# Kernel optimization log

Hardware: AMD Instinct MI355X
Metric: run time of the kernel (lower is better)

## Reference

```python
import jax, jax.numpy as jnp
import numpy as np

EPS = 1e-8
K_KNN = 20

def vn_lin(W, x):
    # W: [Cout, Cin], x: [B, Cin, 3, ...] -> [B, Cout, 3, ...]
    return jnp.einsum('oi,bi...->bo...', W, x)

def vn_relu(Wd, x):
    # VNLeakyReLU with negative_slope=0, share_nonlinearity=False
    d = jnp.einsum('oi,bi...->bo...', Wd, x)
    dot = jnp.sum(x * d, axis=2, keepdims=True)   # sum over 3-vector axis
    dsq = jnp.sum(d * d, axis=2, keepdims=True) + EPS
    return jnp.where(dot >= 0, x, x - (dot / dsq) * d)

def graph_feature_cross(p, k):
    # p: [B, N, 3] -> feat: [B, 3, 3, N, k]
    xx = jnp.sum(p * p, axis=-1)                       # [B,N]
    inner = jnp.einsum('bnd,bmd->bnm', p, p)           # [B,N,N]
    neg_dist = 2.0 * inner - xx[:, :, None] - xx[:, None, :]
    idx = jax.lax.top_k(neg_dist, k)[1]                # [B,N,k] nearest neighbors
    nbrs = jax.vmap(lambda pb, ib: pb[ib])(p, idx)     # [B,N,k,3]
    xr = jnp.broadcast_to(p[:, :, None, :], nbrs.shape)
    cross = jnp.cross(nbrs, xr)                        # [B,N,k,3]
    feat = jnp.stack([nbrs - xr, xr, cross], axis=3)   # [B,N,k,3(ch),3(vec)]
    return jnp.transpose(feat, (0, 3, 4, 1, 2))        # [B,3,3,N,k]

def setup_inputs() -> dict:
    key = jax.random.key(0)
    ks = jax.random.split(key, 9)
    B, N = 4, 2048
    H = 128           # hidden_dim // 3
    C_IN = 2 * H      # 256
    CC = 128          # c_dim // 3
    s_in = 1.0 / np.sqrt(C_IN)
    s_h = 1.0 / np.sqrt(H)
    return {
        'p': jax.random.normal(ks[0], (B, N, 3), dtype=jnp.float32),
        'fc_pos_W': jax.random.normal(ks[1], (C_IN, 3), dtype=jnp.float32) / np.sqrt(3.0),
        'blk_d0': jax.random.normal(ks[2], (5, C_IN, C_IN), dtype=jnp.float32) * s_in,
        'blk_W0': jax.random.normal(ks[3], (5, H, C_IN), dtype=jnp.float32) * s_in,
        'blk_d1': jax.random.normal(ks[4], (5, H, H), dtype=jnp.float32) * s_h,
        'blk_W1': jax.random.normal(ks[5], (5, H, H), dtype=jnp.float32) * s_h,
        'blk_Ws': jax.random.normal(ks[6], (5, H, C_IN), dtype=jnp.float32) * s_in,
        'fc_c_W': jax.random.normal(ks[7], (CC, H), dtype=jnp.float32) * s_h,
        'act_d': jax.random.normal(ks[8], (H, H), dtype=jnp.float32) * s_h,
    }

def reference(p, fc_pos_W, blk_d0, blk_W0, blk_d1, blk_W1, blk_Ws, fc_c_W, act_d):
    feat = graph_feature_cross(p, K_KNN)          # [B,3,3,N,k]
    x = vn_lin(fc_pos_W, feat)                    # [B,256,3,N,k]
    net = jnp.mean(x, axis=-1)                    # mean_pool over k -> [B,256,3,N]

    def block(i, x):
        h = vn_lin(blk_W0[i], vn_relu(blk_d0[i], x))
        dx = vn_lin(blk_W1[i], vn_relu(blk_d1[i], h))
        return vn_lin(blk_Ws[i], x) + dx          # shortcut (size_in != size_out)

    net = block(0, net)                           # [B,128,3,N]
    for i in range(1, 5):
        pooled = jnp.broadcast_to(jnp.mean(net, axis=3, keepdims=True), net.shape)
        net = block(i, jnp.concatenate([net, pooled], axis=1))
    net = jnp.mean(net, axis=3)                   # [B,128,3]
    c = vn_lin(fc_c_W, vn_relu(act_d, net))       # [B,128,3]
    return c.reshape(c.shape[0], -1)              # [B,384]
```

## Files before the change

kernel.cpp:

```cpp
#include <hip/hip_runtime.h>
#include <math.h>

#define N_PTS 2048
#define K_NN  20
#define K_D   10
#define WTOT  819200

typedef unsigned short u16;
typedef unsigned int   u32;
typedef _Float16 f16;
using half8   = __attribute__((ext_vector_type(8))) _Float16;
using floatx4 = __attribute__((ext_vector_type(4))) float;

__device__ __forceinline__ void split2h(float v, f16& h, f16& l) {
    h = (f16)v;
    l = (f16)((v - (float)h) * 1024.0f);
}

__device__ __forceinline__ float neg_dist(float4 q2, float4 c) {
    return fmaf(q2.x, c.x, fmaf(q2.y, c.y, fmaf(q2.z, c.z, -q2.w))) - c.w;
}

__global__ __launch_bounds__(256) void prep_kernel(
    const float* __restrict__ pts, float* __restrict__ m_out,
    const float* __restrict__ bd0, const float* __restrict__ bW0,
    const float* __restrict__ bd1, const float* __restrict__ bW1,
    const float* __restrict__ bWs, u16* __restrict__ Wswz,
    float* __restrict__ nm_acc)
{
    __shared__ float4 sp[N_PTS];
    if (blockIdx.x >= 1024) {
        int i = (blockIdx.x - 1024) * 256 + threadIdx.x;
        if (i >= WTOT) return;
        if (i < 7680) nm_acc[i] = 0.f;
        float v; int base, K, local;
        if (i < 327680)      { int rel = i;          base = (rel/65536)*65536;            local = rel%65536; K = 256; v = bd0[rel]; }
        else if (i < 491520) { int rel = i - 327680; base = 327680 + (rel/32768)*32768;   local = rel%32768; K = 256; v = bW0[rel]; }
        else if (i < 573440) { int rel = i - 491520; base = 491520 + (rel/16384)*16384;   local = rel%16384; K = 128; v = bd1[rel]; }
        else if (i < 655360) { int rel = i - 573440; base = 573440 + (rel/16384)*16384;   local = rel%16384; K = 128; v = bW1[rel]; }
        else                 { int rel = i - 655360; base = 655360 + (rel/32768)*32768;   local = rel%32768; K = 256; v = bWs[rel]; }
        int m = local / K, k = local % K;
        int NKF = K >> 5;
        int mf = m >> 4, r = m & 15;
        int kf = k >> 5, q = (k >> 3) & 3, ii = k & 7;
        int lane = q*16 + r;
        int dst = base + ((mf*NKF + kf)*64 + lane)*8 + ii;
        f16 h, l; split2h(v, h, l);
        f16* W = (f16*)Wswz;
        W[dst] = h; W[WTOT + dst] = l;
        return;
    }

    const int b     = blockIdx.x >> 8;
    const int qbase = (blockIdx.x & 255) << 3;
    const int ql    = threadIdx.x >> 5;
    const int sl    = threadIdx.x & 31;
    const float* pb = pts + (size_t)b * N_PTS * 3;
    for (int i = threadIdx.x; i < N_PTS; i += 256) {
        float x = pb[i*3+0], y = pb[i*3+1], z = pb[i*3+2];
        sp[i] = make_float4(x, y, z, x*x + y*y + z*z);
    }
    __syncthreads();

    const int n = qbase + ql;
    const float4 q = sp[n];
    const float4 q2 = make_float4(2.f*q.x, 2.f*q.y, 2.f*q.z, q.w);

    float t[K_D];
#pragma unroll
    for (int s = 0; s < K_D; ++s) t[s] = -INFINITY;

    for (int j = 0; j < N_PTS/32; ++j) {
        float4 c = sp[j*32 + sl];
        float v = neg_dist(q2, c);
#pragma unroll
        for (int s = 0; s < K_D; ++s) {
            float nx = (s < K_D-1) ? t[s+1] : INFINITY;
            t[s] = fminf(fmaxf(t[s], v), nx);
        }
    }

    float head = t[K_D-1];
    float T = -INFINITY;
#pragma unroll 1
    for (int e = 0; e < K_NN; ++e) {
        float v = head; int w = sl;
#pragma unroll
        for (int off = 1; off < 32; off <<= 1) {
            float vo = __shfl_xor(v, off);
            int   wo = __shfl_xor(w, off);
            bool take = (vo > v) || (vo == v && wo < w);
            v = take ? vo : v;
            w = take ? wo : w;
        }
        T = v;
        if (w == sl) {
#pragma unroll
            for (int s = K_D-1; s > 0; --s) t[s] = t[s-1];
            t[0] = -INFINITY;
            head = t[K_D-1];
        }
    }

    float sx = 0.f, sy = 0.f, sz = 0.f;
    for (int j = 0; j < N_PTS/32; ++j) {
        float4 c = sp[j*32 + sl];
        float v = neg_dist(q2, c);
        if (v >= T) { sx += c.x; sy += c.y; sz += c.z; }
    }
#pragma unroll
    for (int off = 1; off < 32; off <<= 1) {
        sx += __shfl_xor(sx, off);
        sy += __shfl_xor(sy, off);
        sz += __shfl_xor(sz, off);
    }
    if (sl == 0) {
        const float inv = 1.0f / (float)K_NN;
        const int pt = b * N_PTS + n;
        m_out[pt*3+0] = sx * inv;
        m_out[pt*3+1] = sy * inv;
        m_out[pt*3+2] = sz * inv;
    }
}

template<int MF, int JF>
__device__ __forceinline__ void run_gemm_split(
    const f16* __restrict__ Whi, const f16* __restrict__ Wlo, size_t aoff,
    int NKF, int NK, const f16* Blds, int bstride, int lane,
    floatx4 (&acc)[MF][JF], floatx4 (&accL)[MF][JF])
{
    const int l15 = lane & 15;
    const int lq8 = (lane >> 4) * 8;
    half8 Aa[2*MF], Ab[2*MF];

    auto loada = [&](half8* dst, int kf) {
#pragma unroll
        for (int fm = 0; fm < MF; ++fm) {
            size_t fo = aoff + (size_t)(fm*NKF + kf)*512 + (size_t)lane*8;
            dst[fm*2+0] = *(const half8*)(Whi + fo);
            dst[fm*2+1] = *(const half8*)(Wlo + fo);
        }
    };
    auto step = [&](half8* af, int kf) {
        half8 bq[JF];
#pragma unroll
        for (int fj = 0; fj < JF; ++fj)
            bq[fj] = *(const half8*)&Blds[(fj*16 + l15)*bstride + kf*32 + lq8];
#pragma unroll
        for (int fm = 0; fm < MF; ++fm)
#pragma unroll
            for (int fj = 0; fj < JF; ++fj) {
                acc[fm][fj]  = __builtin_amdgcn_mfma_f32_16x16x32_f16(af[fm*2+0], bq[fj], acc[fm][fj], 0, 0, 0);
                accL[fm][fj] = __builtin_amdgcn_mfma_f32_16x16x32_f16(af[fm*2+1], bq[fj], accL[fm][fj], 0, 0, 0);
            }
    };

    loada(Aa, 0);
#pragma unroll 1
    for (int kf = 0; kf < NK; kf += 2) {
        loada(Ab, kf + 1);
        step(Aa, kf);
        if (kf + 2 < NK) loada(Aa, kf + 2);
        step(Ab, kf + 1);
    }
}

template<int MF, int JF>
__device__ __forceinline__ void run_gemm_hi(
    const f16* __restrict__ Whi, size_t aoff,
    int NKF, int NK, const f16* Blds, int bstride, int lane,
    floatx4 (&acc)[MF][JF])
{
    const int l15 = lane & 15;
    const int lq8 = (lane >> 4) * 8;
    half8 Aa[MF], Ab[MF];

    auto loada = [&](half8* dst, int kf) {
#pragma unroll
        for (int fm = 0; fm < MF; ++fm) {
            size_t fo = aoff + (size_t)(fm*NKF + kf)*512 + (size_t)lane*8;
            dst[fm] = *(const half8*)(Whi + fo);
        }
    };
    auto step = [&](half8* af, int kf) {
        half8 bq[JF];
#pragma unroll
        for (int fj = 0; fj < JF; ++fj)
            bq[fj] = *(const half8*)&Blds[(fj*16 + l15)*bstride + kf*32 + lq8];
#pragma unroll
        for (int fm = 0; fm < MF; ++fm)
#pragma unroll
            for (int fj = 0; fj < JF; ++fj)
                acc[fm][fj] = __builtin_amdgcn_mfma_f32_16x16x32_f16(af[fm], bq[fj], acc[fm][fj], 0, 0, 0);
    };

    loada(Aa, 0);
#pragma unroll 1
    for (int kf = 0; kf < NK; kf += 2) {
        loada(Ab, kf + 1);
        step(Aa, kf);
        if (kf + 2 < NK) loada(Aa, kf + 2);
        step(Ab, kf + 1);
    }
}

__device__ __forceinline__ uint2 pack_res(floatx4 a, floatx4 aL) {
    u16 hh[4];
#pragma unroll
    for (int r = 0; r < 4; ++r) {
        f16 hv = (f16)(a[r] + aL[r] * (1.0f/1024.0f));
        hh[r] = *(u16*)&hv;
    }
    uint2 pv;
    pv.x = (u32)hh[0] | ((u32)hh[1] << 16);
    pv.y = (u32)hh[2] | ((u32)hh[3] << 16);
    return pv;
}

__device__ __forceinline__ uint2 pack_hi(floatx4 a) {
    u16 hh[4];
#pragma unroll
    for (int r = 0; r < 4; ++r) {
        f16 hv = (f16)a[r];
        hh[r] = *(u16*)&hv;
    }
    uint2 pv;
    pv.x = (u32)hh[0] | ((u32)hh[1] << 16);
    pv.y = (u32)hh[2] | ((u32)hh[3] << 16);
    return pv;
}

__global__ __launch_bounds__(256, 2) void resblk_kernel(
    const u16* __restrict__ Wswz,
    int offD0, int offW0, int offD1, int offW1, int offWs,
    const f16* __restrict__ netIn, const float* __restrict__ nm_prev,
    const float* __restrict__ pts, const float* __restrict__ m_buf,
    const float* __restrict__ fcW,
    f16* __restrict__ netOut, float* __restrict__ nm_out, int blk0)
{
    __shared__ struct {
        f16 X[48*264];
        union { f16 d[48*264]; float C[48*132]; } Y;
        f16 H[48*136];
    } s;

    const int tid  = threadIdx.x;
    const int jb   = blockIdx.x * 48;
    const int bB   = blockIdx.x >> 7;
    const int lane = tid & 63;
    const int wv   = tid >> 6;
    const f16* Whi = (const f16*)Wswz;
    const f16* Wlo = Whi + WTOT;

    if (blk0) {
        float* Hf = (float*)s.H;
        const int ptbase = blockIdx.x * 16;
        for (int i = tid; i < 768; i += 256) Hf[i] = fcW[i];
        if (tid < 96) Hf[768 + tid] = (tid < 48) ? pts[ptbase*3 + tid]
                                                 : m_buf[ptbase*3 + tid - 48];
        __syncthreads();
#pragma unroll 1
        for (int it = 0; it < 6; ++it) {
            int idx = tid + 256*it;
            int r = idx >> 5;
            int cg = idx & 31;
            int l = r / 3, v = r - l*3;
            float p0 = Hf[768+l*3], p1 = Hf[768+l*3+1], p2 = Hf[768+l*3+2];
            float m0 = Hf[816+l*3], m1 = Hf[816+l*3+1], m2 = Hf[816+l*3+2];
            float pv[3] = {p0,p1,p2}, mv[3] = {m0,m1,m2};
            int v1 = (v==2) ? 0 : v+1;
            int v2 = (v==0) ? 2 : v-1;
            float av = mv[v] - pv[v];
            float bv = pv[v];
            float cv = mv[v1]*pv[v2] - mv[v2]*pv[v1];
            half8 o;
#pragma unroll
            for (int k = 0; k < 8; ++k) {
                int ch = cg*8 + k;
                o[k] = (f16)(Hf[ch*3+0]*av + Hf[ch*3+1]*bv + Hf[ch*3+2]*cv);
            }
            *(half8*)&s.X[r*264 + cg*8] = o;
        }
    } else {
#pragma unroll 1
        for (int it = 0; it < 6; ++it) {
            int idx = tid + 256*it;
            int r = idx >> 5;
            int cg = idx & 31;
            if (cg < 16) {
                uint4 vv = *(const uint4*)(netIn + (size_t)(jb + r)*128 + cg*8);
                *(uint4*)&s.X[r*264 + cg*8] = vv;
            } else {
                int v = r % 3;
                const float* np = nm_prev + (bB*3+v)*128 + (cg-16)*8;
                half8 o;
#pragma unroll
                for (int k = 0; k < 8; ++k) o[k] = (f16)(np[k] * (1.0f/2048.0f));
                *(half8*)&s.X[r*264 + cg*8] = o;
            }
        }
    }
    __syncthreads();

    {
        floatx4 acc[4][3];
#pragma unroll
        for (int a = 0; a < 4; ++a)
#pragma unroll
            for (int b = 0; b < 3; ++b) acc[a][b] = (floatx4){0,0,0,0};
        run_gemm_hi<4,3>(Whi, (size_t)offD0 + (size_t)wv*16384, 8, 8, s.X, 264, lane, acc);
#pragma unroll
        for (int fm = 0; fm < 4; ++fm)
#pragma unroll
            for (int fj = 0; fj < 3; ++fj) {
                int mloc = wv*64 + fm*16 + (lane>>4)*4;
                int jl   = fj*16 + (lane & 15);
                *(uint2*)&s.Y.d[jl*264 + mloc] = pack_hi(acc[fm][fj]);
            }
    }
    __syncthreads();

#pragma unroll 1
    for (int it = 0; it < 2; ++it) {
        int idx = tid + 256*it;
        int l = idx >> 5, cg = idx & 31;
        half8 xa = *(const half8*)&s.X[(l*3+0)*264 + cg*8];
        half8 xb = *(const half8*)&s.X[(l*3+1)*264 + cg*8];
        half8 xc = *(const half8*)&s.X[(l*3+2)*264 + cg*8];
        half8 da = *(const half8*)&s.Y.d[(l*3+0)*264 + cg*8];
        half8 db = *(const half8*)&s.Y.d[(l*3+1)*264 + cg*8];
        half8 dc = *(const half8*)&s.Y.d[(l*3+2)*264 + cg*8];
        half8 ya, yb, yc;
#pragma unroll
        for (int k = 0; k < 8; ++k) {
            float x0 = (float)xa[k], x1 = (float)xb[k], x2 = (float)xc[k];
            float d0 = (float)da[k], d1 = (float)db[k], d2 = (float)dc[k];
            float dot = x0*d0 + x1*d1 + x2*d2;
            float y0, y1, y2;
            if (dot >= 0.f) { y0 = x0; y1 = x1; y2 = x2; }
            else {
                float dsq = d0*d0 + d1*d1 + d2*d2 + 1e-8f;
                float sc = dot / dsq;
                y0 = x0 - sc*d0; y1 = x1 - sc*d1; y2 = x2 - sc*d2;
            }
            ya[k] = (f16)y0; yb[k] = (f16)y1; yc[k] = (f16)y2;
        }
        *(half8*)&s.Y.d[(l*3+0)*264 + cg*8] = ya;
        *(half8*)&s.Y.d[(l*3+1)*264 + cg*8] = yb;
        *(half8*)&s.Y.d[(l*3+2)*264 + cg*8] = yc;
    }
    __syncthreads();

    {
        floatx4 acc[2][3], accL[2][3];
#pragma unroll
        for (int a = 0; a < 2; ++a)
#pragma unroll
            for (int b = 0; b < 3; ++b) { acc[a][b] = (floatx4){0,0,0,0}; accL[a][b] = (floatx4){0,0,0,0}; }
        run_gemm_split<2,3>(Whi, Wlo, (size_t)offW0 + (size_t)wv*8192, 8, 8, s.Y.d, 264, lane, acc, accL);
#pragma unroll
        for (int fm = 0; fm < 2; ++fm)
#pragma unroll
            for (int fj = 0; fj < 3; ++fj) {
                int mloc = wv*32 + fm*16 + (lane>>4)*4;
                int jl   = fj*16 + (lane & 15);
                *(uint2*)&s.H[jl*136 + mloc] = pack_res(acc[fm][fj], accL[fm][fj]);
            }
    }
    __syncthreads();

    {
        floatx4 acc[2][3];
#pragma unroll
        for (int a = 0; a < 2; ++a)
#pragma unroll
            for (int b = 0; b < 3; ++b) acc[a][b] = (floatx4){0,0,0,0};
        run_gemm_hi<2,3>(Whi, (size_t)offD1 + (size_t)wv*4096, 4, 4, s.H, 136, lane, acc);
#pragma unroll
        for (int fm = 0; fm < 2; ++fm)
#pragma unroll
            for (int fj = 0; fj < 3; ++fj) {
                int mloc = wv*32 + fm*16 + (lane>>4)*4;
                int jl   = fj*16 + (lane & 15);
                *(uint2*)&s.Y.d[jl*136 + mloc] = pack_hi(acc[fm][fj]);
            }
    }
    __syncthreads();

    {
        int l = tid >> 4, cg = tid & 15;
        half8 xa = *(const half8*)&s.H[(l*3+0)*136 + cg*8];
        half8 xb = *(const half8*)&s.H[(l*3+1)*136 + cg*8];
        half8 xc = *(const half8*)&s.H[(l*3+2)*136 + cg*8];
        half8 da = *(const half8*)&s.Y.d[(l*3+0)*136 + cg*8];
        half8 db = *(const half8*)&s.Y.d[(l*3+1)*136 + cg*8];
        half8 dc = *(const half8*)&s.Y.d[(l*3+2)*136 + cg*8];
        half8 ya, yb, yc;
#pragma unroll
        for (int k = 0; k < 8; ++k) {
            float x0 = (float)xa[k], x1 = (float)xb[k], x2 = (float)xc[k];
            float d0 = (float)da[k], d1 = (float)db[k], d2 = (float)dc[k];
            float dot = x0*d0 + x1*d1 + x2*d2;
            float y0, y1, y2;
            if (dot >= 0.f) { y0 = x0; y1 = x1; y2 = x2; }
            else {
                float dsq = d0*d0 + d1*d1 + d2*d2 + 1e-8f;
                float sc = dot / dsq;
                y0 = x0 - sc*d0; y1 = x1 - sc*d1; y2 = x2 - sc*d2;
            }
            ya[k] = (f16)y0; yb[k] = (f16)y1; yc[k] = (f16)y2;
        }
        __syncthreads();
        *(half8*)&s.H[(l*3+0)*136 + cg*8] = ya;
        *(half8*)&s.H[(l*3+1)*136 + cg*8] = yb;
        *(half8*)&s.H[(l*3+2)*136 + cg*8] = yc;
    }
    __syncthreads();

    {
        floatx4 acc[2][3], accL[2][3];
#pragma unroll
        for (int a = 0; a < 2; ++a)
#pragma unroll
            for (int b = 0; b < 3; ++b) { acc[a][b] = (floatx4){0,0,0,0}; accL[a][b] = (floatx4){0,0,0,0}; }
        run_gemm_split<2,3>(Whi, Wlo, (size_t)offWs + (size_t)wv*8192, 8, 8, s.X, 264, lane, acc, accL);
        run_gemm_split<2,3>(Whi, Wlo, (size_t)offW1 + (size_t)wv*4096, 4, 4, s.H, 136, lane, acc, accL);
#pragma unroll
        for (int fm = 0; fm < 2; ++fm)
#pragma unroll
            for (int fj = 0; fj < 3; ++fj) {
                int mloc = wv*32 + fm*16 + (lane>>4)*4;
                int jl   = fj*16 + (lane & 15);
                floatx4 res;
#pragma unroll
                for (int r = 0; r < 4; ++r) res[r] = acc[fm][fj][r] + accL[fm][fj][r] * (1.0f/1024.0f);
                u16 hh[4];
#pragma unroll
                for (int r = 0; r < 4; ++r) { f16 hv = (f16)res[r]; hh[r] = *(u16*)&hv; }
                uint2 pv;
                pv.x = (u32)hh[0] | ((u32)hh[1] << 16);
                pv.y = (u32)hh[2] | ((u32)hh[3] << 16);
                *(uint2*)(netOut + (size_t)(jb + jl)*128 + mloc) = pv;
                *(floatx4*)&s.Y.C[jl*132 + mloc] = res;
            }
    }
    __syncthreads();

#pragma unroll 1
    for (int idx = tid; idx < 384; idx += 256) {
        int v = idx >> 7, ch = idx & 127;
        float sum = 0.f;
#pragma unroll 1
        for (int pt = 0; pt < 16; ++pt) sum += s.Y.C[(pt*3+v)*132 + ch];
        atomicAdd(nm_out + (bB*3+v)*128 + ch, sum);
    }
}

__global__ __launch_bounds__(128) void final_kernel(const float* __restrict__ nm_sum,
                                                    const float* __restrict__ act_d,
                                                    const float* __restrict__ fc_c,
                                                    float* __restrict__ out)
{
    const int b = blockIdx.x;
    const int c = threadIdx.x;
    __shared__ float xs[128][3];
    __shared__ float ys[128][3];
    xs[c][0] = nm_sum[(b*3+0)*128 + c] * (1.0f/2048.0f);
    xs[c][1] = nm_sum[(b*3+1)*128 + c] * (1.0f/2048.0f);
    xs[c][2] = nm_sum[(b*3+2)*128 + c] * (1.0f/2048.0f);
    __syncthreads();
    float d0 = 0.f, d1 = 0.f, d2 = 0.f;
    for (int i = 0; i < 128; ++i) {
        float w = act_d[c*128 + i];
        d0 = fmaf(w, xs[i][0], d0);
        d1 = fmaf(w, xs[i][1], d1);
        d2 = fmaf(w, xs[i][2], d2);
    }
    float x0 = xs[c][0], x1 = xs[c][1], x2 = xs[c][2];
    float dot = x0*d0 + x1*d1 + x2*d2;
    float y0, y1, y2;
    if (dot >= 0.f) { y0 = x0; y1 = x1; y2 = x2; }
    else {
        float dsq = d0*d0 + d1*d1 + d2*d2 + 1e-8f;
        float sc = dot / dsq;
        y0 = x0 - sc*d0; y1 = x1 - sc*d1; y2 = x2 - sc*d2;
    }
    ys[c][0] = y0; ys[c][1] = y1; ys[c][2] = y2;
    __syncthreads();
    float o0 = 0.f, o1 = 0.f, o2 = 0.f;
    for (int i = 0; i < 128; ++i) {
        float w = fc_c[c*128 + i];
        o0 = fmaf(w, ys[i][0], o0);
        o1 = fmaf(w, ys[i][1], o1);
        o2 = fmaf(w, ys[i][2], o2);
    }
    out[b*384 + c*3 + 0] = o0;
    out[b*384 + c*3 + 1] = o1;
    out[b*384 + c*3 + 2] = o2;
}

extern "C" void kernel_launch(void* const* d_in, const int* in_sizes, int n_in,
                              void* d_out, int out_size, void* d_ws, size_t ws_size,
                              hipStream_t stream)
{
    const float* p      = (const float*)d_in[0];
    const float* fc_pos = (const float*)d_in[1];
    const float* bd0    = (const float*)d_in[2];
    const float* bW0    = (const float*)d_in[3];
    const float* bd1    = (const float*)d_in[4];
    const float* bW1    = (const float*)d_in[5];
    const float* bWs    = (const float*)d_in[6];
    const float* fc_c   = (const float*)d_in[7];
    const float* act_d  = (const float*)d_in[8];
    float* out = (float*)d_out;

    char* w = (char*)d_ws;
    float* m_buf  = (float*)w;  w += 98304;
    float* nm_acc = (float*)w;  w += 5*1536*4;
    u16*   Wswz   = (u16*)w;    w += (size_t)2*WTOT*2;
    f16*   netA   = (f16*)w;    w += (size_t)24576*128*2;
    f16*   netB   = (f16*)w;    w += (size_t)24576*128*2;

    prep_kernel<<<dim3(1024 + 3200), dim3(256), 0, stream>>>(
        p, m_buf, bd0, bW0, bd1, bW1, bWs, Wswz, nm_acc);

    f16* nIn = netA;
    f16* nOut = netB;
    for (int blk = 0; blk < 5; ++blk) {
        const int offD0 = blk*65536;
        const int offW0 = 327680 + blk*32768;
        const int offD1 = 491520 + blk*16384;
        const int offW1 = 573440 + blk*16384;
        const int offWs = 655360 + blk*32768;
        const float* nmp = (blk == 0) ? nullptr : (nm_acc + (blk-1)*1536);
        resblk_kernel<<<dim3(512), dim3(256), 0, stream>>>(
            Wswz, offD0, offW0, offD1, offW1, offWs,
            (blk == 0) ? netA : nIn, nmp, p, m_buf, fc_pos,
            nOut, nm_acc + blk*1536, (blk == 0) ? 1 : 0);
        f16* tmp = nIn; nIn = nOut; nOut = tmp;
    }

    final_kernel<<<dim3(4), dim3(128), 0, stream>>>(nm_acc + 4*1536, act_d, fc_c, out);

    (void)in_sizes; (void)n_in; (void)out_size; (void)ws_size;
}
```

Before: 242.4 us.

## Fuse final head into last resblock via last-block counter; triple-buffer GEMM loads

The separate final_kernel launch is removed. The last resblock kernel now uses an atomic completion counter so the final block to finish computes the VN-ReLU and linear head, and that launch also skips writing netOut, which nothing reads. The GEMM helpers take K-depth as a template parameter, are fully unrolled, and use a three-deep register buffer for the weight fragments in place of two alternating buffers. The aim is to cut one launch and its gap, drop a global store, and hide weight-load latency better. The cost is a serialized tail in a single block, extra register pressure from the deeper buffer, and reliance on a threadfence/atomic pattern for correctness.

New measurement: 286.4 us. +18.2%, slower.

```diff
diff --git a/kernel.cpp b/kernel.cpp
--- a/kernel.cpp
+++ b/kernel.cpp
@@ -26,13 +26,14 @@
     const float* __restrict__ bd0, const float* __restrict__ bW0,
     const float* __restrict__ bd1, const float* __restrict__ bW1,
     const float* __restrict__ bWs, u16* __restrict__ Wswz,
-    float* __restrict__ nm_acc)
+    float* __restrict__ nm_acc, int* __restrict__ sync_cnt)
 {
     __shared__ float4 sp[N_PTS];
     if (blockIdx.x >= 1024) {
         int i = (blockIdx.x - 1024) * 256 + threadIdx.x;
         if (i >= WTOT) return;
         if (i < 7680) nm_acc[i] = 0.f;
+        if (i == 0) sync_cnt[0] = 0;
         float v; int base, K, local;
         if (i < 327680)      { int rel = i;          base = (rel/65536)*65536;            local = rel%65536; K = 256; v = bd0[rel]; }
         else if (i < 491520) { int rel = i - 327680; base = 327680 + (rel/32768)*32768;   local = rel%32768; K = 256; v = bW0[rel]; }
@@ -123,25 +124,61 @@
     }
 }
 
-template<int MF, int JF>
+template<int MF, int JF, int NK>
+__device__ __forceinline__ void run_gemm_hi(
+    const f16* __restrict__ Whi, size_t aoff,
+    const f16* Blds, int bstride, int lane,
+    floatx4 (&acc)[MF][JF])
+{
+    const int l15 = lane & 15;
+    const int lq8 = (lane >> 4) * 8;
+    half8 buf[3][MF];
+
+    auto loada = [&](half8 (&dst)[MF], int kf) {
+#pragma unroll
+        for (int fm = 0; fm < MF; ++fm)
+            dst[fm] = *(const half8*)(Whi + aoff + (size_t)(fm*NK + kf)*512 + (size_t)lane*8);
+    };
+    auto step = [&](half8 (&af)[MF], int kf) {
+        half8 bq[JF];
+#pragma unroll
+        for (int fj = 0; fj < JF; ++fj)
+            bq[fj] = *(const half8*)&Blds[(fj*16 + l15)*bstride + kf*32 + lq8];
+#pragma unroll
+        for (int fm = 0; fm < MF; ++fm)
+#pragma unroll
+            for (int fj = 0; fj < JF; ++fj)
+                acc[fm][fj] = __builtin_amdgcn_mfma_f32_16x16x32_f16(af[fm], bq[fj], acc[fm][fj], 0, 0, 0);
+    };
+
+    loada(buf[0], 0);
+    if (NK > 1) loada(buf[1], 1);
+#pragma unroll
+    for (int kf = 0; kf < NK; ++kf) {
+        if (kf + 2 < NK) loada(buf[(kf+2)%3], kf+2);
+        step(buf[kf%3], kf);
+    }
+}
+
+template<int MF, int JF, int NK>
 __device__ __forceinline__ void run_gemm_split(
     const f16* __restrict__ Whi, const f16* __restrict__ Wlo, size_t aoff,
-    int NKF, int NK, const f16* Blds, int bstride, int lane,
+    const f16* Blds, int bstride, int lane,
     floatx4 (&acc)[MF][JF], floatx4 (&accL)[MF][JF])
 {
     const int l15 = lane & 15;
     const int lq8 = (lane >> 4) * 8;
-    half8 Aa[2*MF], Ab[2*MF];
-
-    auto loada = [&](half8* dst, int kf) {
+    half8 buf[3][2*MF];
+
+    auto loada = [&](half8 (&dst)[2*MF], int kf) {
 #pragma unroll
         for (int fm = 0; fm < MF; ++fm) {
-            size_t fo = aoff + (size_t)(fm*NKF + kf)*512 + (size_t)lane*8;
+            size_t fo = aoff + (size_t)(fm*NK + kf)*512 + (size_t)lane*8;
             dst[fm*2+0] = *(const half8*)(Whi + fo);
             dst[fm*2+1] = *(const half8*)(Wlo + fo);
         }
     };
-    auto step = [&](half8* af, int kf) {
+    auto step = [&](half8 (&af)[2*MF], int kf) {
         half8 bq[JF];
 #pragma unroll
         for (int fj = 0; fj < JF; ++fj)
@@ -155,52 +192,12 @@
             }
     };
 
-    loada(Aa, 0);
-#pragma unroll 1
-    for (int kf = 0; kf < NK; kf += 2) {
-        loada(Ab, kf + 1);
-        step(Aa, kf);
-        if (kf + 2 < NK) loada(Aa, kf + 2);
-        step(Ab, kf + 1);
-    }
-}
-
-template<int MF, int JF>
-__device__ __forceinline__ void run_gemm_hi(
-    const f16* __restrict__ Whi, size_t aoff,
-    int NKF, int NK, const f16* Blds, int bstride, int lane,
-    floatx4 (&acc)[MF][JF])
-{
-    const int l15 = lane & 15;
-    const int lq8 = (lane >> 4) * 8;
-    half8 Aa[MF], Ab[MF];
-
-    auto loada = [&](half8* dst, int kf) {
-#pragma unroll
-        for (int fm = 0; fm < MF; ++fm) {
-            size_t fo = aoff + (size_t)(fm*NKF + kf)*512 + (size_t)lane*8;
-            dst[fm] = *(const half8*)(Whi + fo);
-        }
-    };
-    auto step = [&](half8* af, int kf) {
-        half8 bq[JF];
-#pragma unroll
-        for (int fj = 0; fj < JF; ++fj)
-            bq[fj] = *(const half8*)&Blds[(fj*16 + l15)*bstride + kf*32 + lq8];
-#pragma unroll
-        for (int fm = 0; fm < MF; ++fm)
-#pragma unroll
-            for (int fj = 0; fj < JF; ++fj)
-                acc[fm][fj] = __builtin_amdgcn_mfma_f32_16x16x32_f16(af[fm], bq[fj], acc[fm][fj], 0, 0, 0);
-    };
-
-    loada(Aa, 0);
-#pragma unroll 1
-    for (int kf = 0; kf < NK; kf += 2) {
-        loada(Ab, kf + 1);
-        step(Aa, kf);
-        if (kf + 2 < NK) loada(Aa, kf + 2);
-        step(Ab, kf + 1);
+    loada(buf[0], 0);
+    if (NK > 1) loada(buf[1], 1);
+#pragma unroll
+    for (int kf = 0; kf < NK; ++kf) {
+        if (kf + 2 < NK) loada(buf[(kf+2)%3], kf+2);
+        step(buf[kf%3], kf);
     }
 }
 
@@ -236,13 +233,17 @@
     const f16* __restrict__ netIn, const float* __restrict__ nm_prev,
     const float* __restrict__ pts, const float* __restrict__ m_buf,
     const float* __restrict__ fcW,
-    f16* __restrict__ netOut, float* __restrict__ nm_out, int blk0)
+    f16* __restrict__ netOut, float* __restrict__ nm_out, int blk0,
+    int do_head, int* __restrict__ sync_cnt,
+    const float* __restrict__ act_d, const float* __restrict__ fc_c,
+    float* __restrict__ out)
 {
     __shared__ struct {
         f16 X[48*264];
         union { f16 d[48*264]; float C[48*132]; } Y;
         f16 H[48*136];
     } s;
+    __shared__ int lastFlag;
 
     const int tid  = threadIdx.x;
     const int jb   = blockIdx.x * 48;
@@ -265,14 +266,13 @@
             int r = idx >> 5;
             int cg = idx & 31;
             int l = r / 3, v = r - l*3;
-            float p0 = Hf[768+l*3], p1 = Hf[768+l*3+1], p2 = Hf[768+l*3+2];
-            float m0 = Hf[816+l*3], m1 = Hf[816+l*3+1], m2 = Hf[816+l*3+2];
-            float pv[3] = {p0,p1,p2}, mv[3] = {m0,m1,m2};
+            float pv0[3] = {Hf[768+l*3], Hf[768+l*3+1], Hf[768+l*3+2]};
+            float mv0[3] = {Hf[816+l*3], Hf[816+l*3+1], Hf[816+l*3+2]};
             int v1 = (v==2) ? 0 : v+1;
             int v2 = (v==0) ? 2 : v-1;
-            float av = mv[v] - pv[v];
-            float bv = pv[v];
-            float cv = mv[v1]*pv[v2] - mv[v2]*pv[v1];
+            float av = mv0[v] - pv0[v];
+            float bv = pv0[v];
+            float cv = mv0[v1]*pv0[v2] - mv0[v2]*pv0[v1];
             half8 o;
 #pragma unroll
             for (int k = 0; k < 8; ++k) {
@@ -308,7 +308,7 @@
         for (int a = 0; a < 4; ++a)
 #pragma unroll
             for (int b = 0; b < 3; ++b) acc[a][b] = (floatx4){0,0,0,0};
-        run_gemm_hi<4,3>(Whi, (size_t)offD0 + (size_t)wv*16384, 8, 8, s.X, 264, lane, acc);
+        run_gemm_hi<4,3,8>(Whi, (size_t)offD0 + (size_t)wv*16384, s.X, 264, lane, acc);
 #pragma unroll
         for (int fm = 0; fm < 4; ++fm)
 #pragma unroll
@@ -357,7 +357,7 @@
         for (int a = 0; a < 2; ++a)
 #pragma unroll
             for (int b = 0; b < 3; ++b) { acc[a][b] = (floatx4){0,0,0,0}; accL[a][b] = (floatx4){0,0,0,0}; }
-        run_gemm_split<2,3>(Whi, Wlo, (size_t)offW0 + (size_t)wv*8192, 8, 8, s.Y.d, 264, lane, acc, accL);
+        run_gemm_split<2,3,8>(Whi, Wlo, (size_t)offW0 + (size_t)wv*8192, s.Y.d, 264, lane, acc, accL);
 #pragma unroll
         for (int fm = 0; fm < 2; ++fm)
 #pragma unroll
@@ -375,7 +375,7 @@
         for (int a = 0; a < 2; ++a)
 #pragma unroll
             for (int b = 0; b < 3; ++b) acc[a][b] = (floatx4){0,0,0,0};
-        run_gemm_hi<2,3>(Whi, (size_t)offD1 + (size_t)wv*4096, 4, 4, s.H, 136, lane, acc);
+        run_gemm_hi<2,3,4>(Whi, (size_t)offD1 + (size_t)wv*4096, s.H, 136, lane, acc);
 #pragma unroll
         for (int fm = 0; fm < 2; ++fm)
 #pragma unroll
@@ -423,8 +423,8 @@
         for (int a = 0; a < 2; ++a)
 #pragma unroll
             for (int b = 0; b < 3; ++b) { acc[a][b] = (floatx4){0,0,0,0}; accL[a][b] = (floatx4){0,0,0,0}; }
-        run_gemm_split<2,3>(Whi, Wlo, (size_t)offWs + (size_t)wv*8192, 8, 8, s.X, 264, lane, acc, accL);
-        run_gemm_split<2,3>(Whi, Wlo, (size_t)offW1 + (size_t)wv*4096, 4, 4, s.H, 136, lane, acc, accL);
+        run_gemm_split<2,3,8>(Whi, Wlo, (size_t)offWs + (size_t)wv*8192, s.X, 264, lane, acc, accL);
+        run_gemm_split<2,3,4>(Whi, Wlo, (size_t)offW1 + (size_t)wv*4096, s.H, 136, lane, acc, accL);
 #pragma unroll
         for (int fm = 0; fm < 2; ++fm)
 #pragma unroll
@@ -434,13 +434,15 @@
                 floatx4 res;
 #pragma unroll
                 for (int r = 0; r < 4; ++r) res[r] = acc[fm][fj][r] + accL[fm][fj][r] * (1.0f/1024.0f);
-                u16 hh[4];
-#pragma unroll
-                for (int r = 0; r < 4; ++r) { f16 hv = (f16)res[r]; hh[r] = *(u16*)&hv; }
-                uint2 pv;
-                pv.x = (u32)hh[0] | ((u32)hh[1] << 16);
-                pv.y = (u32)hh[2] | ((u32)hh[3] << 16);
-                *(uint2*)(netOut + (size_t)(jb + jl)*128 + mloc) = pv;
+                if (!do_head) {
+                    u16 hh[4];
+#pragma unroll
+                    for (int r = 0; r < 4; ++r) { f16 hv = (f16)res[r]; hh[r] = *(u16*)&hv; }
+                    uint2 pv;
+                    pv.x = (u32)hh[0] | ((u32)hh[1] << 16);
+                    pv.y = (u32)hh[2] | ((u32)hh[3] << 16);
+                    *(uint2*)(netOut + (size_t)(jb + jl)*128 + mloc) = pv;
+                }
                 *(floatx4*)&s.Y.C[jl*132 + mloc] = res;
             }
     }
@@ -454,49 +456,59 @@
         for (int pt = 0; pt < 16; ++pt) sum += s.Y.C[(pt*3+v)*132 + ch];
         atomicAdd(nm_out + (bB*3+v)*128 + ch, sum);
     }
-}
-
-__global__ __launch_bounds__(128) void final_kernel(const float* __restrict__ nm_sum,
-                                                    const float* __restrict__ act_d,
-                                                    const float* __restrict__ fc_c,
-                                                    float* __restrict__ out)
-{
-    const int b = blockIdx.x;
-    const int c = threadIdx.x;
-    __shared__ float xs[128][3];
-    __shared__ float ys[128][3];
-    xs[c][0] = nm_sum[(b*3+0)*128 + c] * (1.0f/2048.0f);
-    xs[c][1] = nm_sum[(b*3+1)*128 + c] * (1.0f/2048.0f);
-    xs[c][2] = nm_sum[(b*3+2)*128 + c] * (1.0f/2048.0f);
-    __syncthreads();
-    float d0 = 0.f, d1 = 0.f, d2 = 0.f;
-    for (int i = 0; i < 128; ++i) {
-        float w = act_d[c*128 + i];
-        d0 = fmaf(w, xs[i][0], d0);
-        d1 = fmaf(w, xs[i][1], d1);
-        d2 = fmaf(w, xs[i][2], d2);
-    }
-    float x0 = xs[c][0], x1 = xs[c][1], x2 = xs[c][2];
-    float dot = x0*d0 + x1*d1 + x2*d2;
-    float y0, y1, y2;
-    if (dot >= 0.f) { y0 = x0; y1 = x1; y2 = x2; }
-    else {
-        float dsq = d0*d0 + d1*d1 + d2*d2 + 1e-8f;
-        float sc = dot / dsq;
-        y0 = x0 - sc*d0; y1 = x1 - sc*d1; y2 = x2 - sc*d2;
-    }
-    ys[c][0] = y0; ys[c][1] = y1; ys[c][2] = y2;
-    __syncthreads();
-    float o0 = 0.f, o1 = 0.f, o2 = 0.f;
-    for (int i = 0; i < 128; ++i) {
-        float w = fc_c[c*128 + i];
-        o0 = fmaf(w, ys[i][0], o0);
-        o1 = fmaf(w, ys[i][1], o1);
-        o2 = fmaf(w, ys[i][2], o2);
-    }
-    out[b*384 + c*3 + 0] = o0;
-    out[b*384 + c*3 + 1] = o1;
-    out[b*384 + c*3 + 2] = o2;
+
+    if (do_head) {
+        __threadfence();
+        if (tid == 0) lastFlag = (atomicAdd(sync_cnt, 1) == 511) ? 1 : 0;
+        __syncthreads();
+        if (lastFlag) {
+            __threadfence();
+            float* xs = (float*)&s.X[0];
+            float* ys = xs + 768;
+            const int c = tid & 127;
+            const int half = tid >> 7;
+            float* nm_sum = nm_out;
+#pragma unroll 1
+            for (int rep = 0; rep < 2; ++rep) {
+                int b = half + rep*2;
+                float* x = xs + half*384;
+                float* y = ys + half*384;
+                x[c*3+0] = atomicAdd(&nm_sum[(b*3+0)*128 + c], 0.0f) * (1.0f/2048.0f);
+                x[c*3+1] = atomicAdd(&nm_sum[(b*3+1)*128 + c], 0.0f) * (1.0f/2048.0f);
+                x[c*3+2] = atomicAdd(&nm_sum[(b*3+2)*128 + c], 0.0f) * (1.0f/2048.0f);
+                __syncthreads();
+                float d0 = 0.f, d1 = 0.f, d2 = 0.f;
+                for (int i = 0; i < 128; ++i) {
+                    float w = act_d[c*128 + i];
+                    d0 = fmaf(w, x[i*3+0], d0);
+                    d1 = fmaf(w, x[i*3+1], d1);
+                    d2 = fmaf(w, x[i*3+2], d2);
+                }
+                float x0 = x[c*3+0], x1 = x[c*3+1], x2 = x[c*3+2];
+                float dot = x0*d0 + x1*d1 + x2*d2;
+                float y0, y1, y2;
+                if (dot >= 0.f) { y0 = x0; y1 = x1; y2 = x2; }
+                else {
+                    float dsq = d0*d0 + d1*d1 + d2*d2 + 1e-8f;
+                    float sc = dot / dsq;
+                    y0 = x0 - sc*d0; y1 = x1 - sc*d1; y2 = x2 - sc*d2;
+                }
+                y[c*3+0] = y0; y[c*3+1] = y1; y[c*3+2] = y2;
+                __syncthreads();
+                float o0 = 0.f, o1 = 0.f, o2 = 0.f;
+                for (int i = 0; i < 128; ++i) {
+                    float w = fc_c[c*128 + i];
+                    o0 = fmaf(w, y[i*3+0], o0);
+                    o1 = fmaf(w, y[i*3+1], o1);
+                    o2 = fmaf(w, y[i*3+2], o2);
+                }
+                out[b*384 + c*3 + 0] = o0;
+                out[b*384 + c*3 + 1] = o1;
+                out[b*384 + c*3 + 2] = o2;
+                __syncthreads();
+            }
+        }
+    }
 }
 
 extern "C" void kernel_launch(void* const* d_in, const int* in_sizes, int n_in,
@@ -515,14 +527,15 @@
     float* out = (float*)d_out;
 
     char* w = (char*)d_ws;
-    float* m_buf  = (float*)w;  w += 98304;
-    float* nm_acc = (float*)w;  w += 5*1536*4;
-    u16*   Wswz   = (u16*)w;    w += (size_t)2*WTOT*2;
-    f16*   netA   = (f16*)w;    w += (size_t)24576*128*2;
-    f16*   netB   = (f16*)w;    w += (size_t)24576*128*2;
+    float* m_buf    = (float*)w;  w += 98304;
+    float* nm_acc   = (float*)w;  w += 5*1536*4;
+    int*   sync_cnt = (int*)w;    w += 16;
+    u16*   Wswz     = (u16*)w;    w += (size_t)2*WTOT*2;
+    f16*   netA     = (f16*)w;    w += (size_t)24576*128*2;
+    f16*   netB     = (f16*)w;    w += (size_t)24576*128*2;
 
     prep_kernel<<<dim3(1024 + 3200), dim3(256), 0, stream>>>(
-        p, m_buf, bd0, bW0, bd1, bW1, bWs, Wswz, nm_acc);
+        p, m_buf, bd0, bW0, bd1, bW1, bWs, Wswz, nm_acc, sync_cnt);
 
     f16* nIn = netA;
     f16* nOut = netB;
@@ -536,11 +549,10 @@
         resblk_kernel<<<dim3(512), dim3(256), 0, stream>>>(
             Wswz, offD0, offW0, offD1, offW1, offWs,
             (blk == 0) ? netA : nIn, nmp, p, m_buf, fc_pos,
-            nOut, nm_acc + blk*1536, (blk == 0) ? 1 : 0);
+            nOut, nm_acc + blk*1536, (blk == 0) ? 1 : 0,
+            (blk == 4) ? 1 : 0, sync_cnt, act_d, fc_c, out);
         f16* tmp = nIn; nIn = nOut; nOut = tmp;
     }
 
-    final_kernel<<<dim3(4), dim3(128), 0, stream>>>(nm_acc + 4*1536, act_d, fc_c, out);
-
     (void)in_sizes; (void)n_in; (void)out_size; (void)ws_size;
 }
```

## Drop H LDS buffer, reuse X, hoist shortcut GEMM, skip final net store

Applied to the files above, without the earlier changes.

The separate H shared-memory buffer is removed. The shortcut GEMM (Ws·X) now runs early into persistent accumulators, which frees X so the h and relu outputs can be stored there. This cuts LDS per block so launch bounds can ask for 3 blocks per CU. The last block also skips writing netOut, since only its mean is consumed. The trade-off is that the shortcut accumulators (acc4/accL4) stay live across the middle GEMMs, which raises register pressure and may cause spills under the tighter occupancy bound.

Result: no change. 241.2 us (-0.5%).

```diff
diff --git a/kernel.cpp b/kernel.cpp
--- a/kernel.cpp
+++ b/kernel.cpp
@@ -124,24 +124,61 @@
 }
 
 template<int MF, int JF>
+__device__ __forceinline__ void run_gemm_hi(
+    const f16* __restrict__ Whi, size_t aoff,
+    int NK, const f16* Blds, int bstride, int lane,
+    floatx4 (&acc)[MF][JF])
+{
+    const int l15 = lane & 15;
+    const int lq8 = (lane >> 4) * 8;
+    half8 Aa[MF], Ab[MF];
+
+    auto loada = [&](half8 (&dst)[MF], int kf) {
+#pragma unroll
+        for (int fm = 0; fm < MF; ++fm)
+            dst[fm] = *(const half8*)(Whi + aoff + (size_t)(fm*NK + kf)*512 + (size_t)lane*8);
+    };
+    auto step = [&](half8 (&af)[MF], int kf) {
+        half8 bq[JF];
+#pragma unroll
+        for (int fj = 0; fj < JF; ++fj)
+            bq[fj] = *(const half8*)&Blds[(fj*16 + l15)*bstride + kf*32 + lq8];
+#pragma unroll
+        for (int fm = 0; fm < MF; ++fm)
+#pragma unroll
+            for (int fj = 0; fj < JF; ++fj)
+                acc[fm][fj] = __builtin_amdgcn_mfma_f32_16x16x32_f16(af[fm], bq[fj], acc[fm][fj], 0, 0, 0);
+    };
+
+    loada(Aa, 0);
+#pragma unroll 1
+    for (int kf = 0; kf < NK; kf += 2) {
+        loada(Ab, kf + 1);
+        step(Aa, kf);
+        if (kf + 2 < NK) loada(Aa, kf + 2);
+        step(Ab, kf + 1);
+    }
+}
+
+template<int MF, int JF>
 __device__ __forceinline__ void run_gemm_split(
     const f16* __restrict__ Whi, const f16* __restrict__ Wlo, size_t aoff,
-    int NKF, int NK, const f16* Blds, int bstride, int lane,
+    int NK, const f16* Blds, int bstride, int lane,
     floatx4 (&acc)[MF][JF], floatx4 (&accL)[MF][JF])
 {
     const int l15 = lane & 15;
     const int lq8 = (lane >> 4) * 8;
     half8 Aa[2*MF], Ab[2*MF];
 
-    auto loada = [&](half8* dst, int kf) {
+    auto loada = [&](half8 (&dst)[2*MF], int kf) {
 #pragma unroll
         for (int fm = 0; fm < MF; ++fm) {
-            size_t fo = aoff + (size_t)(fm*NKF + kf)*512 + (size_t)lane*8;
+            size_t fo = aoff + (size_t)(fm*NK + kf)*512 + (size_t)lane*8;
             dst[fm*2+0] = *(const half8*)(Whi + fo);
             dst[fm*2+1] = *(const half8*)(Wlo + fo);
         }
     };
-    auto step = [&](half8* af, int kf) {
+    auto step = [&](half8 (&af)[2*MF], int kf) {
         half8 bq[JF];
 #pragma unroll
         for (int fj = 0; fj < JF; ++fj)
@@ -165,45 +202,6 @@
     }
 }
 
-template<int MF, int JF>
-__device__ __forceinline__ void run_gemm_hi(
-    const f16* __restrict__ Whi, size_t aoff,
-    int NKF, int NK, const f16* Blds, int bstride, int lane,
-    floatx4 (&acc)[MF][JF])
-{
-    const int l15 = lane & 15;
-    const int lq8 = (lane >> 4) * 8;
-    half8 Aa[MF], Ab[MF];
-
-    auto loada = [&](half8* dst, int kf) {
-#pragma unroll
-        for (int fm = 0; fm < MF; ++fm) {
-            size_t fo = aoff + (size_t)(fm*NKF + kf)*512 + (size_t)lane*8;
-            dst[fm] = *(const half8*)(Whi + fo);
-        }
-    };
-    auto step = [&](half8* af, int kf) {
-        half8 bq[JF];
-#pragma unroll
-        for (int fj = 0; fj < JF; ++fj)
-            bq[fj] = *(const half8*)&Blds[(fj*16 + l15)*bstride + kf*32 + lq8];
-#pragma unroll
-        for (int fm = 0; fm < MF; ++fm)
-#pragma unroll
-            for (int fj = 0; fj < JF; ++fj)
-                acc[fm][fj] = __builtin_amdgcn_mfma_f32_16x16x32_f16(af[fm], bq[fj], acc[fm][fj], 0, 0, 0);
-    };
-
-    loada(Aa, 0);
-#pragma unroll 1
-    for (int kf = 0; kf < NK; kf += 2) {
-        loada(Ab, kf + 1);
-        step(Aa, kf);
-        if (kf + 2 < NK) loada(Aa, kf + 2);
-        step(Ab, kf + 1);
-    }
-}
-
 __device__ __forceinline__ uint2 pack_res(floatx4 a, floatx4 aL) {
     u16 hh[4];
 #pragma unroll
@@ -230,18 +228,18 @@
     return pv;
 }
 
-__global__ __launch_bounds__(256, 2) void resblk_kernel(
+__global__ __launch_bounds__(256, 3) void resblk_kernel(
     const u16* __restrict__ Wswz,
     int offD0, int offW0, int offD1, int offW1, int offWs,
     const f16* __restrict__ netIn, const float* __restrict__ nm_prev,
     const float* __restrict__ pts, const float* __restrict__ m_buf,
     const float* __restrict__ fcW,
-    f16* __restrict__ netOut, float* __restrict__ nm_out, int blk0)
+    f16* __restrict__ netOut, float* __restrict__ nm_out, int blk0,
+    int skip_store)
 {
     __shared__ struct {
         f16 X[48*264];
         union { f16 d[48*264]; float C[48*132]; } Y;
-        f16 H[48*136];
     } s;
 
     const int tid  = threadIdx.x;
@@ -253,7 +251,7 @@
     const f16* Wlo = Whi + WTOT;
 
     if (blk0) {
-        float* Hf = (float*)s.H;
+        float* Hf = (float*)s.Y.C;
         const int ptbase = blockIdx.x * 16;
         for (int i = tid; i < 768; i += 256) Hf[i] = fcW[i];
         if (tid < 96) Hf[768 + tid] = (tid < 48) ? pts[ptbase*3 + tid]
@@ -265,14 +263,13 @@
             int r = idx >> 5;
             int cg = idx & 31;
             int l = r / 3, v = r - l*3;
-            float p0 = Hf[768+l*3], p1 = Hf[768+l*3+1], p2 = Hf[768+l*3+2];
-            float m0 = Hf[816+l*3], m1 = Hf[816+l*3+1], m2 = Hf[816+l*3+2];
-            float pv[3] = {p0,p1,p2}, mv[3] = {m0,m1,m2};
+            float pv0[3] = {Hf[768+l*3], Hf[768+l*3+1], Hf[768+l*3+2]};
+            float mv0[3] = {Hf[816+l*3], Hf[816+l*3+1], Hf[816+l*3+2]};
             int v1 = (v==2) ? 0 : v+1;
             int v2 = (v==0) ? 2 : v-1;
-            float av = mv[v] - pv[v];
-            float bv = pv[v];
-            float cv = mv[v1]*pv[v2] - mv[v2]*pv[v1];
+            float av = mv0[v] - pv0[v];
+            float bv = pv0[v];
+            float cv = mv0[v1]*pv0[v2] - mv0[v2]*pv0[v1];
             half8 o;
 #pragma unroll
             for (int k = 0; k < 8; ++k) {
@@ -302,13 +299,19 @@
     }
     __syncthreads();
 
+    floatx4 acc4[2][3], accL4[2][3];
+#pragma unroll
+    for (int a = 0; a < 2; ++a)
+#pragma unroll
+        for (int b = 0; b < 3; ++b) { acc4[a][b] = (floatx4){0,0,0,0}; accL4[a][b] = (floatx4){0,0,0,0}; }
+
     {
         floatx4 acc[4][3];
 #pragma unroll
         for (int a = 0; a < 4; ++a)
 #pragma unroll
             for (int b = 0; b < 3; ++b) acc[a][b] = (floatx4){0,0,0,0};
-        run_gemm_hi<4,3>(Whi, (size_t)offD0 + (size_t)wv*16384, 8, 8, s.X, 264, lane, acc);
+        run_gemm_hi<4,3>(Whi, (size_t)offD0 + (size_t)wv*16384, 8, s.X, 264, lane, acc);
 #pragma unroll
         for (int fm = 0; fm < 4; ++fm)
 #pragma unroll
@@ -319,6 +322,8 @@
             }
     }
     __syncthreads();
+
+    run_gemm_split<2,3>(Whi, Wlo, (size_t)offWs + (size_t)wv*8192, 8, s.X, 264, lane, acc4, accL4);
 
 #pragma unroll 1
     for (int it = 0; it < 2; ++it) {
@@ -357,14 +362,14 @@
         for (int a = 0; a < 2; ++a)
 #pragma unroll
             for (int b = 0; b < 3; ++b) { acc[a][b] = (floatx4){0,0,0,0}; accL[a][b] = (floatx4){0,0,0,0}; }
-        run_gemm_split<2,3>(Whi, Wlo, (size_t)offW0 + (size_t)wv*8192, 8, 8, s.Y.d, 264, lane, acc, accL);
+        run_gemm_split<2,3>(Whi, Wlo, (size_t)offW0 + (size_t)wv*8192, 8, s.Y.d, 264, lane, acc, accL);
 #pragma unroll
         for (int fm = 0; fm < 2; ++fm)
 #pragma unroll
             for (int fj = 0; fj < 3; ++fj) {
                 int mloc = wv*32 + fm*16 + (lane>>4)*4;
                 int jl   = fj*16 + (lane & 15);
-                *(uint2*)&s.H[jl*136 + mloc] = pack_res(acc[fm][fj], accL[fm][fj]);
+                *(uint2*)&s.X[jl*136 + mloc] = pack_res(acc[fm][fj], accL[fm][fj]);
             }
     }
     __syncthreads();
@@ -375,7 +380,7 @@
         for (int a = 0; a < 2; ++a)
 #pragma unroll
             for (int b = 0; b < 3; ++b) acc[a][b] = (floatx4){0,0,0,0};
-        run_gemm_hi<2,3>(Whi, (size_t)offD1 + (size_t)wv*4096, 4, 4, s.H, 136, lane, acc);
+        run_gemm_hi<2,3>(Whi, (size_t)offD1 + (size_t)wv*4096, 4, s.X, 136, lane, acc);
 #pragma unroll
         for (int fm = 0; fm < 2; ++fm)
 #pragma unroll
@@ -389,9 +394,9 @@
 
     {
         int l = tid >> 4, cg = tid & 15;
-        half8 xa = *(const half8*)&s.H[(l*3+0)*136 + cg*8];
-        half8 xb = *(const half8*)&s.H[(l*3+1)*136 + cg*8];
-        half8 xc = *(const half8*)&s.H[(l*3+2)*136 + cg*8];
+        half8 xa = *(const half8*)&s.X[(l*3+0)*136 + cg*8];
+        half8 xb = *(const half8*)&s.X[(l*3+1)*136 + cg*8];
+        half8 xc = *(const half8*)&s.X[(l*3+2)*136 + cg*8];
         half8 da = *(const half8*)&s.Y.d[(l*3+0)*136 + cg*8];
         half8 db = *(const half8*)&s.Y.d[(l*3+1)*136 + cg*8];
         half8 dc = *(const half8*)&s.Y.d[(l*3+2)*136 + cg*8];
@@ -411,29 +416,24 @@
             ya[k] = (f16)y0; yb[k] = (f16)y1; yc[k] = (f16)y2;
         }
         __syncthreads();
-        *(half8*)&s.H[(l*3+0)*136 + cg*8] = ya;
-        *(half8*)&s.H[(l*3+1)*136 + cg*8] = yb;
-        *(half8*)&s.H[(l*3+2)*136 + cg*8] = yc;
-    }
-    __syncthreads();
-
-    {
-        floatx4 acc[2][3], accL[2][3];
-#pragma unroll
-        for (int a = 0; a < 2; ++a)
-#pragma unroll
-            for (int b = 0; b < 3; ++b) { acc[a][b] = (floatx4){0,0,0,0}; accL[a][b] = (floatx4){0,0,0,0}; }
-        run_gemm_split<2,3>(Whi, Wlo, (size_t)offWs + (size_t)wv*8192, 8, 8, s.X, 264, lane, acc, accL);
-        run_gemm_split<2,3>(Whi, Wlo, (size_t)offW1 + (size_t)wv*4096, 4, 4, s.H, 136, lane, acc, accL);
-#pragma unroll
-        for (int fm = 0; fm < 2; ++fm)
-#pragma unroll
-            for (int fj = 0; fj < 3; ++fj) {
-                int mloc = wv*32 + fm*16 + (lane>>4)*4;
-                int jl   = fj*16 + (lane & 15);
-                floatx4 res;
-#pragma unroll
-                for (int r = 0; r < 4; ++r) res[r] = acc[fm][fj][r] + accL[fm][fj][r] * (1.0f/1024.0f);
+        *(half8*)&s.X[(l*3+0)*136 + cg*8] = ya;
+        *(half8*)&s.X[(l*3+1)*136 + cg*8] = yb;
+        *(half8*)&s.X[(l*3+2)*136 + cg*8] = yc;
+    }
+    __syncthreads();
+
+    run_gemm_split<2,3>(Whi, Wlo, (size_t)offW1 + (size_t)wv*4096, 4, s.X, 136, lane, acc4, accL4);
+
+#pragma unroll
+    for (int fm = 0; fm < 2; ++fm)
+#pragma unroll
+        for (int fj = 0; fj < 3; ++fj) {
+            int mloc = wv*32 + fm*16 + (lane>>4)*4;
+            int jl   = fj*16 + (lane & 15);
+            floatx4 res;
+#pragma unroll
+            for (int r = 0; r < 4; ++r) res[r] = acc4[fm][fj][r] + accL4[fm][fj][r] * (1.0f/1024.0f);
+            if (!skip_store) {
                 u16 hh[4];
 #pragma unroll
                 for (int r = 0; r < 4; ++r) { f16 hv = (f16)res[r]; hh[r] = *(u16*)&hv; }
@@ -441,9 +441,9 @@
                 pv.x = (u32)hh[0] | ((u32)hh[1] << 16);
                 pv.y = (u32)hh[2] | ((u32)hh[3] << 16);
                 *(uint2*)(netOut + (size_t)(jb + jl)*128 + mloc) = pv;
-                *(floatx4*)&s.Y.C[jl*132 + mloc] = res;
-            }
-    }
+            }
+            *(floatx4*)&s.Y.C[jl*132 + mloc] = res;
+        }
     __syncthreads();
 
 #pragma unroll 1
@@ -536,7 +536,8 @@
         resblk_kernel<<<dim3(512), dim3(256), 0, stream>>>(
             Wswz, offD0, offW0, offD1, offW1, offWs,
             (blk == 0) ? netA : nIn, nmp, p, m_buf, fc_pos,
-            nOut, nm_acc + blk*1536, (blk == 0) ? 1 : 0);
+            nOut, nm_acc + blk*1536, (blk == 0) ? 1 : 0,
+            (blk == 4) ? 1 : 0);
         f16* tmp = nIn; nIn = nOut; nOut = tmp;
     }
 
```
